# Optimization experiments

Measured on AMD Instinct MI355X. Metric: run time of the kernel, lower is better.

Reference implementation:

```python
import jax, jax.numpy as jnp
import numpy as np

RADIUS = 0.1
DILATION = 0.05
KERNEL_SIZE = 3  # per dim, ndim=3 -> ncells=27
NDIM = 3


def _cell_offsets():
    # Kernel cell center offsets relative to the query location.
    idx = jnp.stack(jnp.meshgrid(*([jnp.arange(KERNEL_SIZE)] * NDIM), indexing='ij'), axis=-1)
    idx = idx.reshape(-1, NDIM).astype(jnp.float32)  # [ncells, D]
    return (idx - (KERNEL_SIZE - 1) / 2.0) * DILATION


def setup_inputs() -> dict:
    key = jax.random.key(0)
    k1, k2, k3, k4, k5, k6 = jax.random.split(key, 6)
    B, N, M, K, C, O = 2, 8192, 8192, 32, 16, 16
    ncells = KERNEL_SIZE ** NDIM
    qlocs = jax.random.uniform(k1, (B, M, NDIM), dtype=jnp.float32)
    locs = jax.random.uniform(k2, (B, N, NDIM), dtype=jnp.float32)
    data = jax.random.normal(k3, (B, N, C), dtype=jnp.float32)
    neighbors = jax.random.randint(k4, (B, M, K), 0, N, dtype=jnp.int32)
    weight = jax.random.normal(k5, (O, C, ncells), dtype=jnp.float32) * 0.1
    bias = jax.random.normal(k6, (O,), dtype=jnp.float32) * 0.1
    return {"qlocs": qlocs, "locs": locs, "data": data,
            "neighbors": neighbors, "weight": weight, "bias": bias}


def reference(qlocs, locs, data, neighbors, weight, bias):
    # qlocs: [B,M,D], locs: [B,N,D], data: [B,N,C]
    # neighbors: [B,M,K] (-1 padded), weight: [O,C,ncells], bias: [O]
    valid = neighbors >= 0                      # [B,M,K]
    nid = jnp.where(valid, neighbors, 0)
    # Gather neighbor locations/features per batch.
    nlocs = jax.vmap(lambda l, n: l[n])(locs, nid)   # [B,M,K,D]
    ndata = jax.vmap(lambda d, n: d[n])(data, nid)   # [B,M,K,C]

    off = _cell_offsets()                            # [ncells, D]
    # Cell centers around each query point: [B,M,ncells,D]
    centers = qlocs[:, :, None, :] + off[None, None, :, :]
    # Distance from each cell center to each neighbor: [B,M,ncells,K]
    diff = centers[:, :, :, None, :] - nlocs[:, :, None, :, :]
    d = jnp.sqrt(jnp.sum(diff * diff, axis=-1) + 1e-12)
    q = d / RADIUS
    # 'default' SPH smoothing kernel: compact support, (1 - d/H)^3 inside radius.
    kv = jnp.where((q < 1.0) & valid[:, :, None, :], (1.0 - q) ** 3, 0.0)  # [B,M,ncells,K]

    # Per-cell SPH-weighted feature accumulation: [B,M,C,ncells]
    acc = jnp.einsum('bmek,bmkc->bmce', kv, ndata)
    # Contract with conv weights: [B,M,O]
    out = jnp.einsum('bmce,oce->bmo', acc, weight) + bias[None, None, :]
    return out
```

## Files before the change

### kernel.cpp

```cpp
#include <hip/hip_runtime.h>
#include <math.h>

#define NP 8192
#define KN 32
#define CH 16
#define OCH 16
#define NCELL 27
#define EPAD 36

#define THR2 0.0349f

__global__ __launch_bounds__(512, 6) void convsp_kernel(
    const float* __restrict__ qlocs,
    const float* __restrict__ locs,
    const float* __restrict__ data,
    const int*   __restrict__ neighbors,
    const float* __restrict__ weight,
    const float* __restrict__ bias,
    float* __restrict__ out)
{
    __shared__ float  wlds[OCH * CH * EPAD];
    __shared__ float4 offs4[32];

    const int tid  = threadIdx.x;
    const int lane = tid & 63;
    const int c    = lane & 15;
    const int h    = lane >> 4;
    const int pt   = blockIdx.x * 8 + (tid >> 6);
    const int b    = pt >> 13;

    int   nid = neighbors[pt * KN + (lane & 31)];
    float qx = qlocs[pt * 3 + 0];
    float qy = qlocs[pt * 3 + 1];
    float qz = qlocs[pt * 3 + 2];
    float bi = bias[c];

    const float4* w4g = (const float4*)weight;
    for (int idx = tid; idx < (OCH * CH * NCELL) / 4; idx += 512) {
        float4 w = w4g[idx];
        int f = idx * 4;
        int r0 = (f + 0) / NCELL, e0 = (f + 0) - r0 * NCELL;
        int r1 = (f + 1) / NCELL, e1 = (f + 1) - r1 * NCELL;
        int r2 = (f + 2) / NCELL, e2 = (f + 2) - r2 * NCELL;
        int r3 = (f + 3) / NCELL, e3 = (f + 3) - r3 * NCELL;
        wlds[r0 * EPAD + e0] = w.x;
        wlds[r1 * EPAD + e1] = w.y;
        wlds[r2 * EPAD + e2] = w.z;
        wlds[r3 * EPAD + e3] = w.w;
    }
    for (int idx = tid; idx < OCH * CH * 9; idx += 512) {
        int row = idx / 9;
        int e   = 27 + (idx - row * 9);
        wlds[row * EPAD + e] = 0.0f;
    }
    if (tid < 32) {
        int e = tid;
        float ox = (e < NCELL) ? (float)(e / 9 - 1) * 0.05f : 0.0f;
        float oy = (e < NCELL) ? (float)((e / 3) % 3 - 1) * 0.05f : 0.0f;
        float oz = (e < NCELL) ? (float)(e % 3 - 1) * 0.05f : 0.0f;
        offs4[tid] = make_float4(ox, oy, oz, 0.0f);
    }

    int gaddr = (b * NP + max(nid, 0)) * 3;
    float lx = locs[gaddr], ly = locs[gaddr + 1], lz = locs[gaddr + 2];

    __syncthreads();

    float oxr[8], oyr[8], ozr[8];
    #pragma unroll
    for (int i = 0; i < 8; ++i) {
        float4 o4 = offs4[h * 8 + i];
        oxr[i] = o4.x; oyr[i] = o4.y; ozr[i] = o4.z;
    }

    float dx = qx - lx, dy = qy - ly, dz = qz - lz;
    bool hit = (nid >= 0) && (dx * dx + dy * dy + dz * dz < THR2);
    unsigned int mask = (unsigned int)__ballot(hit);

    float acc[8];
    #pragma unroll
    for (int i = 0; i < 8; ++i) acc[i] = 0.0f;

    unsigned int mrem = mask;
    while (mrem) {
        int k = __builtin_ctz(mrem);
        mrem &= mrem - 1;

        int   nk = __shfl(nid, k, 64);
        float nx = __shfl(lx,  k, 64);
        float ny = __shfl(ly,  k, 64);
        float nz = __shfl(lz,  k, 64);

        float ndc = data[(b * NP + nk) * CH + c];

        float dqx = qx - nx, dqy = qy - ny, dqz = qz - nz;

        #pragma unroll
        for (int i = 0; i < 8; ++i) {
            float ex = dqx + oxr[i], ey = dqy + oyr[i], ez = dqz + ozr[i];
            float t = fmaf(ex, ex, fmaf(ey, ey, ez * ez)) + 1e-12f;
            float u = fmaxf(fmaf(-10.0f, __builtin_amdgcn_sqrtf(t), 1.0f), 0.0f);
            acc[i] += (u * u) * (u * ndc);
        }
    }

    float r = 0.0f;
    if (mask) {
        const float* wrow = &wlds[c * EPAD + h * 8];

        float vv[8];
        #pragma unroll
        for (int j = 0; j < 8; ++j) {
            const float4* wA = (const float4*)(wrow + (2 * j)     * CH * EPAD);
            const float4* wB = (const float4*)(wrow + (2 * j + 1) * CH * EPAD);
            float4 a0 = wA[0], a1 = wA[1];
            float4 b0 = wB[0], b1 = wB[1];
            float pA = a0.x*acc[0] + a0.y*acc[1] + a0.z*acc[2] + a0.w*acc[3]
                     + a1.x*acc[4] + a1.y*acc[5] + a1.z*acc[6] + a1.w*acc[7];
            float pB = b0.x*acc[0] + b0.y*acc[1] + b0.z*acc[2] + b0.w*acc[3]
                     + b1.x*acc[4] + b1.y*acc[5] + b1.z*acc[6] + b1.w*acc[7];
            int bit = c & 1;
            float keep = bit ? pB : pA;
            float send = bit ? pA : pB;
            vv[j] = keep + __shfl_xor(send, 1, 64);
        }
        #pragma unroll
        for (int i = 1; i < 4; ++i) {
            int bit = (c >> i) & 1;
            #pragma unroll
            for (int j = 0; j < (8 >> i); ++j) {
                float keep = bit ? vv[2 * j + 1] : vv[2 * j];
                float send = bit ? vv[2 * j]     : vv[2 * j + 1];
                vv[j] = keep + __shfl_xor(send, 1 << i, 64);
            }
        }
        r = vv[0];
        r += __shfl_xor(r, 16, 64);
        r += __shfl_xor(r, 32, 64);
    }

    if (h == 0) out[pt * OCH + c] = r + bi;
}

extern "C" void kernel_launch(void* const* d_in, const int* in_sizes, int n_in,
                              void* d_out, int out_size, void* d_ws, size_t ws_size,
                              hipStream_t stream) {
    const float* qlocs     = (const float*)d_in[0];
    const float* locs      = (const float*)d_in[1];
    const float* data      = (const float*)d_in[2];
    const int*   neighbors = (const int*)d_in[3];
    const float* weight    = (const float*)d_in[4];
    const float* bias      = (const float*)d_in[5];
    float*       out       = (float*)d_out;

    const int BM = in_sizes[0] / 3;
    dim3 grid(BM / 8), block(512);
    hipLaunchKernelGGL(convsp_kernel, grid, block, 0, stream,
                       qlocs, locs, data, neighbors, weight, bias, out);
}
```

Before: 20.91 us.

## Process four query points per wavefront and overlap weight staging with neighbor accumulation

Each wavefront now handles four query points instead of one, so a block covers 32 points and the grid shrinks fourfold. Each 16-lane group loads one point's 32 neighbors and builds its hit mask, then the whole wave walks each point's hits in turn. The weight-to-LDS staging is therefore amortized over more points. Weight global loads are issued up front, the LDS stores and `__syncthreads` are deferred until after the neighbor accumulation, and cell offsets are computed arithmetically instead of via LDS. The LDS weight reads in the output contraction are shared across the four points. This raises register use (4x8 accumulators and reduction buffers), and the occupancy hint drops from 6 to 4.

```diff
diff --git a/kernel.cpp b/kernel.cpp
--- a/kernel.cpp
+++ b/kernel.cpp
@@ -10,7 +10,7 @@
 
 #define THR2 0.0349f
 
-__global__ __launch_bounds__(512, 6) void convsp_kernel(
+__global__ __launch_bounds__(512, 4) void convsp_kernel(
     const float* __restrict__ qlocs,
     const float* __restrict__ locs,
     const float* __restrict__ data,
@@ -19,127 +19,153 @@
     const float* __restrict__ bias,
     float* __restrict__ out)
 {
-    __shared__ float  wlds[OCH * CH * EPAD];
-    __shared__ float4 offs4[32];
+    __shared__ float wlds[OCH * CH * EPAD];
 
     const int tid  = threadIdx.x;
     const int lane = tid & 63;
     const int c    = lane & 15;
     const int h    = lane >> 4;
-    const int pt   = blockIdx.x * 8 + (tid >> 6);
-    const int b    = pt >> 13;
-
-    int   nid = neighbors[pt * KN + (lane & 31)];
-    float qx = qlocs[pt * 3 + 0];
-    float qy = qlocs[pt * 3 + 1];
-    float qz = qlocs[pt * 3 + 2];
-    float bi = bias[c];
+    const int wv   = tid >> 6;
+    const int pt0  = blockIdx.x * 32 + wv * 4;
+    const int b    = blockIdx.x >> 8;
+    const int bN   = b * NP;
 
     const float4* w4g = (const float4*)weight;
-    for (int idx = tid; idx < (OCH * CH * NCELL) / 4; idx += 512) {
-        float4 w = w4g[idx];
-        int f = idx * 4;
-        int r0 = (f + 0) / NCELL, e0 = (f + 0) - r0 * NCELL;
-        int r1 = (f + 1) / NCELL, e1 = (f + 1) - r1 * NCELL;
-        int r2 = (f + 2) / NCELL, e2 = (f + 2) - r2 * NCELL;
-        int r3 = (f + 3) / NCELL, e3 = (f + 3) - r3 * NCELL;
-        wlds[r0 * EPAD + e0] = w.x;
-        wlds[r1 * EPAD + e1] = w.y;
-        wlds[r2 * EPAD + e2] = w.z;
-        wlds[r3 * EPAD + e3] = w.w;
-    }
+    float4 wr0 = w4g[tid];
+    float4 wr1 = w4g[tid + 512];
+    float4 wr2 = w4g[tid + 1024];
+    float4 wr3 = (tid < 192) ? w4g[tid + 1536] : make_float4(0.f, 0.f, 0.f, 0.f);
+
+    const int ptq = pt0 + h;
+    const float qx = qlocs[ptq * 3 + 0];
+    const float qy = qlocs[ptq * 3 + 1];
+    const float qz = qlocs[ptq * 3 + 2];
+    const float bi = bias[c];
+    const int nid0 = neighbors[ptq * KN + c];
+    const int nid1 = neighbors[ptq * KN + 16 + c];
+    int g0 = (bN + max(nid0, 0)) * 3;
+    int g1 = (bN + max(nid1, 0)) * 3;
+    float l0x = locs[g0], l0y = locs[g0 + 1], l0z = locs[g0 + 2];
+    float l1x = locs[g1], l1y = locs[g1 + 1], l1z = locs[g1 + 2];
+
     for (int idx = tid; idx < OCH * CH * 9; idx += 512) {
         int row = idx / 9;
-        int e   = 27 + (idx - row * 9);
-        wlds[row * EPAD + e] = 0.0f;
+        wlds[row * EPAD + 27 + (idx - row * 9)] = 0.0f;
     }
-    if (tid < 32) {
-        int e = tid;
-        float ox = (e < NCELL) ? (float)(e / 9 - 1) * 0.05f : 0.0f;
-        float oy = (e < NCELL) ? (float)((e / 3) % 3 - 1) * 0.05f : 0.0f;
-        float oz = (e < NCELL) ? (float)(e % 3 - 1) * 0.05f : 0.0f;
-        offs4[tid] = make_float4(ox, oy, oz, 0.0f);
-    }
-
-    int gaddr = (b * NP + max(nid, 0)) * 3;
-    float lx = locs[gaddr], ly = locs[gaddr + 1], lz = locs[gaddr + 2];
-
-    __syncthreads();
 
     float oxr[8], oyr[8], ozr[8];
     #pragma unroll
     for (int i = 0; i < 8; ++i) {
-        float4 o4 = offs4[h * 8 + i];
-        oxr[i] = o4.x; oyr[i] = o4.y; ozr[i] = o4.z;
+        int e  = h * 8 + i;
+        int d9 = (e * 228) >> 11;
+        int d3 = (e * 683) >> 11;
+        oxr[i] = (float)(d9 - 1) * 0.05f;
+        oyr[i] = (float)(d3 - 3 * d9 - 1) * 0.05f;
+        ozr[i] = (float)(e - 3 * d3 - 1) * 0.05f;
     }
 
-    float dx = qx - lx, dy = qy - ly, dz = qz - lz;
-    bool hit = (nid >= 0) && (dx * dx + dy * dy + dz * dz < THR2);
-    unsigned int mask = (unsigned int)__ballot(hit);
+    float dx0 = qx - l0x, dy0 = qy - l0y, dz0 = qz - l0z;
+    float dx1 = qx - l1x, dy1 = qy - l1y, dz1 = qz - l1z;
+    bool hit0 = (nid0 >= 0) && (dx0 * dx0 + dy0 * dy0 + dz0 * dz0 < THR2);
+    bool hit1 = (nid1 >= 0) && (dx1 * dx1 + dy1 * dy1 + dz1 * dz1 < THR2);
+    unsigned long long bl0 = __ballot(hit0);
+    unsigned long long bl1 = __ballot(hit1);
 
-    float acc[8];
+    float acc[4][8];
     #pragma unroll
-    for (int i = 0; i < 8; ++i) acc[i] = 0.0f;
+    for (int p = 0; p < 4; ++p)
+        #pragma unroll
+        for (int i = 0; i < 8; ++i) acc[p][i] = 0.0f;
 
-    unsigned int mrem = mask;
-    while (mrem) {
-        int k = __builtin_ctz(mrem);
-        mrem &= mrem - 1;
+    #pragma unroll
+    for (int p = 0; p < 4; ++p) {
+        unsigned int mp = (unsigned int)((bl0 >> (p * 16)) & 0xFFFFull)
+                        | ((unsigned int)((bl1 >> (p * 16)) & 0xFFFFull) << 16);
+        while (mp) {
+            int k = __builtin_ctz(mp);
+            mp &= mp - 1;
+            int  src = p * 16 + (k & 15);
+            bool lo  = (k < 16);
+            int   nk  = __shfl(lo ? nid0 : nid1, src, 64);
+            float dqx = __shfl(lo ? dx0  : dx1,  src, 64);
+            float dqy = __shfl(lo ? dy0  : dy1,  src, 64);
+            float dqz = __shfl(lo ? dz0  : dz1,  src, 64);
 
-        int   nk = __shfl(nid, k, 64);
-        float nx = __shfl(lx,  k, 64);
-        float ny = __shfl(ly,  k, 64);
-        float nz = __shfl(lz,  k, 64);
+            float ndc = data[(bN + nk) * CH + c];
 
-        float ndc = data[(b * NP + nk) * CH + c];
-
-        float dqx = qx - nx, dqy = qy - ny, dqz = qz - nz;
-
-        #pragma unroll
-        for (int i = 0; i < 8; ++i) {
-            float ex = dqx + oxr[i], ey = dqy + oyr[i], ez = dqz + ozr[i];
-            float t = fmaf(ex, ex, fmaf(ey, ey, ez * ez)) + 1e-12f;
-            float u = fmaxf(fmaf(-10.0f, __builtin_amdgcn_sqrtf(t), 1.0f), 0.0f);
-            acc[i] += (u * u) * (u * ndc);
+            #pragma unroll
+            for (int i = 0; i < 8; ++i) {
+                float ex = dqx + oxr[i], ey = dqy + oyr[i], ez = dqz + ozr[i];
+                float t  = fmaf(ex, ex, fmaf(ey, ey, ez * ez)) + 1e-12f;
+                float u  = fmaxf(fmaf(-10.0f, __builtin_amdgcn_sqrtf(t), 1.0f), 0.0f);
+                acc[p][i] += (u * u) * (u * ndc);
+            }
         }
     }
 
-    float r = 0.0f;
-    if (mask) {
+    #pragma unroll
+    for (int j = 0; j < 4; ++j) {
+        if (j < 3 || tid < 192) {
+            float4 w = (j == 0) ? wr0 : (j == 1) ? wr1 : (j == 2) ? wr2 : wr3;
+            int f  = (tid + j * 512) * 4;
+            int r0 = (f + 0) / NCELL, e0 = (f + 0) - r0 * NCELL;
+            int r1 = (f + 1) / NCELL, e1 = (f + 1) - r1 * NCELL;
+            int r2 = (f + 2) / NCELL, e2 = (f + 2) - r2 * NCELL;
+            int r3 = (f + 3) / NCELL, e3 = (f + 3) - r3 * NCELL;
+            wlds[r0 * EPAD + e0] = w.x;
+            wlds[r1 * EPAD + e1] = w.y;
+            wlds[r2 * EPAD + e2] = w.z;
+            wlds[r3 * EPAD + e3] = w.w;
+        }
+    }
+    __syncthreads();
+
+    float r0s = 0.f, r1s = 0.f, r2s = 0.f, r3s = 0.f;
+    if (bl0 | bl1) {
         const float* wrow = &wlds[c * EPAD + h * 8];
-
-        float vv[8];
+        const int bit0 = c & 1;
+        float vv[4][8];
         #pragma unroll
         for (int j = 0; j < 8; ++j) {
             const float4* wA = (const float4*)(wrow + (2 * j)     * CH * EPAD);
             const float4* wB = (const float4*)(wrow + (2 * j + 1) * CH * EPAD);
             float4 a0 = wA[0], a1 = wA[1];
             float4 b0 = wB[0], b1 = wB[1];
-            float pA = a0.x*acc[0] + a0.y*acc[1] + a0.z*acc[2] + a0.w*acc[3]
-                     + a1.x*acc[4] + a1.y*acc[5] + a1.z*acc[6] + a1.w*acc[7];
-            float pB = b0.x*acc[0] + b0.y*acc[1] + b0.z*acc[2] + b0.w*acc[3]
-                     + b1.x*acc[4] + b1.y*acc[5] + b1.z*acc[6] + b1.w*acc[7];
-            int bit = c & 1;
-            float keep = bit ? pB : pA;
-            float send = bit ? pA : pB;
-            vv[j] = keep + __shfl_xor(send, 1, 64);
+            #pragma unroll
+            for (int p = 0; p < 4; ++p) {
+                float pA = a0.x*acc[p][0] + a0.y*acc[p][1] + a0.z*acc[p][2] + a0.w*acc[p][3]
+                         + a1.x*acc[p][4] + a1.y*acc[p][5] + a1.z*acc[p][6] + a1.w*acc[p][7];
+                float pB = b0.x*acc[p][0] + b0.y*acc[p][1] + b0.z*acc[p][2] + b0.w*acc[p][3]
+                         + b1.x*acc[p][4] + b1.y*acc[p][5] + b1.z*acc[p][6] + b1.w*acc[p][7];
+                float keep = bit0 ? pB : pA;
+                float send = bit0 ? pA : pB;
+                vv[p][j] = keep + __shfl_xor(send, 1, 64);
+            }
         }
         #pragma unroll
         for (int i = 1; i < 4; ++i) {
             int bit = (c >> i) & 1;
             #pragma unroll
-            for (int j = 0; j < (8 >> i); ++j) {
-                float keep = bit ? vv[2 * j + 1] : vv[2 * j];
-                float send = bit ? vv[2 * j]     : vv[2 * j + 1];
-                vv[j] = keep + __shfl_xor(send, 1 << i, 64);
+            for (int p = 0; p < 4; ++p) {
+                #pragma unroll
+                for (int j = 0; j < (8 >> i); ++j) {
+                    float keep = bit ? vv[p][2 * j + 1] : vv[p][2 * j];
+                    float send = bit ? vv[p][2 * j]     : vv[p][2 * j + 1];
+                    vv[p][j] = keep + __shfl_xor(send, 1 << i, 64);
+                }
             }
         }
-        r = vv[0];
-        r += __shfl_xor(r, 16, 64);
-        r += __shfl_xor(r, 32, 64);
+        r0s = vv[0][0]; r0s += __shfl_xor(r0s, 16, 64); r0s += __shfl_xor(r0s, 32, 64);
+        r1s = vv[1][0]; r1s += __shfl_xor(r1s, 16, 64); r1s += __shfl_xor(r1s, 32, 64);
+        r2s = vv[2][0]; r2s += __shfl_xor(r2s, 16, 64); r2s += __shfl_xor(r2s, 32, 64);
+        r3s = vv[3][0]; r3s += __shfl_xor(r3s, 16, 64); r3s += __shfl_xor(r3s, 32, 64);
     }
 
-    if (h == 0) out[pt * OCH + c] = r + bi;
+    float rw = r0s;
+    if (h == 1) rw = r1s;
+    if (h == 2) rw = r2s;
+    if (h == 3) rw = r3s;
+    out[pt0 * CH + lane] = rw + bi;
 }
 
 extern "C" void kernel_launch(void* const* d_in, const int* in_sizes, int n_in,
@@ -154,7 +180,7 @@
     float*       out       = (float*)d_out;
 
     const int BM = in_sizes[0] / 3;
-    dim3 grid(BM / 8), block(512);
+    dim3 grid(BM / 32), block(512);
     hipLaunchKernelGGL(convsp_kernel, grid, block, 0, stream,
                        qlocs, locs, data, neighbors, weight, bias, out);
 }
```

Result: faster. 18.62 us (-11.0%).
